# Kernel tuning notes

Measured on AMD Instinct MI355X. Metric: run time of the kernel, lower is better.

Reference implementation:

```python
import jax, jax.numpy as jnp
import numpy as np

K = 15          # n_clusters
D = 64          # dim_latent
M = 100         # number of w samples
LOG_2PI = float(np.log(2.0 * np.pi))

# state -> (cluster A, cluster B) edge endpoints, upper-triangular incl. diagonal
_A, _B = np.nonzero(np.triu(np.ones((K, K))))  # each [S], S = K*(K+1)/2 = 120


def setup_inputs() -> dict:
    key = jax.random.key(0)
    k1, k2, k3 = jax.random.split(key, 3)
    z = jax.random.normal(k1, (4096, 1, D), dtype=jnp.float32)      # [B, L, D]
    pi = jax.random.normal(k2, (1, K * (K + 1) // 2), dtype=jnp.float32)  # [1, S]
    mu = jax.random.uniform(k3, (D, K), dtype=jnp.float32, minval=-1.0, maxval=1.0)
    return {"z": z, "pi": pi, "mu": mu}


def reference(z, pi, mu):
    # w grid: [M]
    w = jnp.arange(M, dtype=z.dtype) / M
    # interpolated component means mu_sm[d, s, m] = mu[d,A[s]]*w[m] + mu[d,B[s]]*(1-w[m])
    mu_sm = mu[:, _A, None] * w + mu[:, _B, None] * (1.0 - w)   # [D, S, M]
    log_pi = jnp.log(jax.nn.softmax(pi, axis=-1) + 1e-30)       # [1, S]

    # squared distance via ||z||^2 - 2 z.mu + ||mu||^2 (avoids [B,L,D,S,M] materialization)
    zz = jnp.sum(z * z, axis=-1)                                # [B, L]
    cross = jnp.einsum('bld,dsm->blsm', z, mu_sm)               # [B, L, S, M]
    mm = jnp.sum(mu_sm * mu_sm, axis=0)                         # [S, M]
    sq = zz[..., None, None] - 2.0 * cross + mm                 # [B, L, S, M]

    log_p_zc_w = (-0.5 * D * LOG_2PI
                  + log_pi[0][None, None, :, None]
                  - 0.5 * sq)                                   # [B, L, S, M]
    log_p_z_L = jax.scipy.special.logsumexp(log_p_zc_w, axis=(2, 3))  # [B, L]
    log_p_z = jnp.mean(log_p_z_L) - jnp.log(jnp.asarray(M, z.dtype))
    return log_p_z
```

## Files before the change

### kernel.cpp

```cpp
#include <hip/hip_runtime.h>
#include <math.h>
#include <float.h>

#define D 64
#define K 15
#define S 120
#define MNUM 100
#define C0 (-58.81206612509905f)
#define L2E 1.4426950408889634f
#define INV_L2E 0.6931471805599453f

static __device__ __forceinline__ float fexp2(float x) {
    return __builtin_amdgcn_exp2f(x);
}


__global__ __launch_bounds__(128) void gmm_setup(const float* __restrict__ pi,
                                                 const float* __restrict__ mu,
                                                 float* __restrict__ wsf,
                                                 int* __restrict__ wsi) {
    __shared__ float red[2];
    __shared__ float bcast;
    const int t = threadIdx.x;
    const int wid = t >> 6;

    float p = (t < S) ? pi[t] : -FLT_MAX;
    float mx = p;
    for (int off = 32; off; off >>= 1) mx = fmaxf(mx, __shfl_down(mx, off));
    if ((t & 63) == 0) red[wid] = mx;
    __syncthreads();
    if (t == 0) bcast = fmaxf(red[0], red[1]);
    __syncthreads();
    mx = bcast;
    __syncthreads();

    float e = (t < S) ? __expf(p - mx) : 0.f;
    float se = e;
    for (int off = 32; off; off >>= 1) se += __shfl_down(se, off);
    if ((t & 63) == 0) red[wid] = se;
    __syncthreads();
    if (t == 0) bcast = red[0] + red[1];
    __syncthreads();
    se = bcast;

    if (t < S) {
        float sm = e / se;
        float logpi = logf(sm + 1e-30f);

        int i = 0, rem = t;
        while (rem >= K - i) { rem -= K - i; ++i; }
        int j = i + rem;

        float aa = 0.f, ab = 0.f, bb = 0.f;
        for (int d = 0; d < D; ++d) {
            float ma = mu[d * K + i];
            float mb = mu[d * K + j];
            aa = fmaf(ma, ma, aa);
            ab = fmaf(ma, mb, ab);
            bb = fmaf(mb, mb, bb);
        }
        float q0 = bb;
        float q1 = 2.f * (ab - bb);
        float q2 = aa - 2.f * ab + bb;

        wsf[t]       = C0 + logpi - 0.5f * q0;
        wsf[128 + t] = -0.5f * q1;
        wsf[256 + t] = -0.5f * q2;
        wsi[t]       = i;
        wsi[128 + t] = j;
    }
}

__global__ __launch_bounds__(256) void gmm_main(const float* __restrict__ z,
                                                const float* __restrict__ mu,
                                                const float* __restrict__ wsf,
                                                const int* __restrict__ wsi,
                                                float* __restrict__ lse) {
    __shared__ float zsh[4][D];
    const int t = threadIdx.x;
    const int lane = t & 63;
    const int wv = t >> 6;
    const int b = (blockIdx.x << 2) + wv;

    float zval = z[b * D + lane];
    zsh[wv][lane] = zval;
    float zz = zval * zval;
    #pragma unroll
    for (int off = 32; off; off >>= 1) zz += __shfl_xor(zz, off);
    __syncthreads();

    const int g = lane >> 4;
    const int kk = lane & 15;
    const int kkc = (kk < K) ? kk : (K - 1);
    const float* zw = &zsh[wv][g * 16];
    float cpart = 0.f;
    #pragma unroll
    for (int i = 0; i < 16; ++i)
        cpart = fmaf(zw[i], mu[(g * 16 + i) * K + kkc], cpart);
    cpart += __shfl_xor(cpart, 16);
    cpart += __shfl_xor(cpart, 32);

    const int s1 = lane;
    const int s2 = lane + 64;
    const bool v2 = (s2 < S);
    const int s2c = v2 ? s2 : (S - 1);

    float cA1 = __shfl(cpart, wsi[s1]);
    float cB1 = __shfl(cpart, wsi[128 + s1]);
    float cA2 = __shfl(cpart, wsi[s2c]);
    float cB2 = __shfl(cpart, wsi[128 + s2c]);

    float T01 = wsf[s1] + cB1 - 0.5f * zz;
    float T11 = wsf[128 + s1] + (cA1 - cB1);
    float T21 = wsf[256 + s1];
    float T02 = v2 ? (wsf[s2c] + cB2 - 0.5f * zz) : -1e30f;
    float T12 = wsf[128 + s2c] + (cA2 - cB2);
    float T22 = wsf[256 + s2c];

    float bnd = fmaxf(T01, fmaf(0.99f, fmaf(0.99f, T21, T11), T01));
    if (T21 < 0.f) {
        float wv1 = fminf(fmaxf(-T11 / (2.f * T21), 0.f), 0.99f);
        bnd = fmaxf(bnd, fmaf(wv1, fmaf(wv1, T21, T11), T01));
    }
    if (v2) {
        float b2 = fmaxf(T02, fmaf(0.99f, fmaf(0.99f, T22, T12), T02));
        if (T22 < 0.f) {
            float wv2 = fminf(fmaxf(-T12 / (2.f * T22), 0.f), 0.99f);
            b2 = fmaxf(b2, fmaf(wv2, fmaf(wv2, T22, T12), T02));
        }
        bnd = fmaxf(bnd, b2);
    }
    #pragma unroll
    for (int off = 32; off; off >>= 1) bnd = fmaxf(bnd, __shfl_xor(bnd, off));
    const float Mb = bnd;

    const float u01 = (T01 - Mb) * L2E, u11 = T11 * L2E, u21 = T21 * L2E;
    const float u02 = (T02 - Mb) * L2E, u12 = T12 * L2E, u22 = T22 * L2E;

    float sumA = 0.f, sumB = 0.f;
    float w = 0.f;
    #pragma unroll 10
    for (int m = 0; m < 100; ++m) {
        sumA += fexp2(fmaf(w, fmaf(w, u21, u11), u01));
        sumB += fexp2(fmaf(w, fmaf(w, u22, u12), u02));
        w += 0.01f;
    }
    float ssum = sumA + sumB;
    #pragma unroll
    for (int off = 32; off; off >>= 1) ssum += __shfl_xor(ssum, off);

    if (lane == 0)
        lse[b] = Mb + __builtin_amdgcn_logf(ssum) * INV_L2E;
}

__global__ __launch_bounds__(256) void gmm_reduce(const float* __restrict__ lse,
                                                  float* __restrict__ out) {
    __shared__ float red[4];
    const int t = threadIdx.x;
    float s = 0.f;
    #pragma unroll
    for (int i = 0; i < 16; ++i) s += lse[t + i * 256];
    #pragma unroll
    for (int off = 32; off; off >>= 1) s += __shfl_down(s, off);
    if ((t & 63) == 0) red[t >> 6] = s;
    __syncthreads();
    if (t == 0)
        out[0] = (red[0] + red[1] + red[2] + red[3]) * (1.0f / 4096.0f)
                 - logf((float)MNUM);
}

extern "C" void kernel_launch(void* const* d_in, const int* in_sizes, int n_in,
                              void* d_out, int out_size, void* d_ws, size_t ws_size,
                              hipStream_t stream) {
    const float* z  = (const float*)d_in[0];
    const float* pi = (const float*)d_in[1];
    const float* mu = (const float*)d_in[2];
    float* out = (float*)d_out;

    float* wsf = (float*)d_ws;
    int*   wsi = (int*)(wsf + 384);
    float* lse = wsf + 1024;

    gmm_setup<<<1, 128, 0, stream>>>(pi, mu, wsf, wsi);
    gmm_main<<<1024, 256, 0, stream>>>(z, mu, wsf, wsi, lse);
    gmm_reduce<<<1, 256, 0, stream>>>(lse, out);
}
```

Measured before the change: 72.58 us.

## Replace per-sample exp2 with multiplicative recurrence from grid midpoint

The 100 exp2 evaluations per state are replaced by a geometric recurrence: the Gaussian-in-w term is computed as products of precomputed ratio factors, stepping outward from w=0.5 in both directions, so only four exp2 calls per state remain. Division in the bound computation is replaced by a hardware reciprocal. This removes transcendental throughput cost from the inner loop but accumulates rounding error over 50 chained multiplies and may underflow or overflow for extreme exponents.

```diff
diff --git a/kernel.cpp b/kernel.cpp
--- a/kernel.cpp
+++ b/kernel.cpp
@@ -119,13 +119,13 @@
 
     float bnd = fmaxf(T01, fmaf(0.99f, fmaf(0.99f, T21, T11), T01));
     if (T21 < 0.f) {
-        float wv1 = fminf(fmaxf(-T11 / (2.f * T21), 0.f), 0.99f);
+        float wv1 = fminf(fmaxf(-T11 * 0.5f * __builtin_amdgcn_rcpf(T21), 0.f), 0.99f);
         bnd = fmaxf(bnd, fmaf(wv1, fmaf(wv1, T21, T11), T01));
     }
     if (v2) {
         float b2 = fmaxf(T02, fmaf(0.99f, fmaf(0.99f, T22, T12), T02));
         if (T22 < 0.f) {
-            float wv2 = fminf(fmaxf(-T12 / (2.f * T22), 0.f), 0.99f);
+            float wv2 = fminf(fmaxf(-T12 * 0.5f * __builtin_amdgcn_rcpf(T22), 0.f), 0.99f);
             b2 = fmaxf(b2, fmaf(wv2, fmaf(wv2, T22, T12), T02));
         }
         bnd = fmaxf(bnd, b2);
@@ -134,18 +134,34 @@
     for (int off = 32; off; off >>= 1) bnd = fmaxf(bnd, __shfl_xor(bnd, off));
     const float Mb = bnd;
 
-    const float u01 = (T01 - Mb) * L2E, u11 = T11 * L2E, u21 = T21 * L2E;
-    const float u02 = (T02 - Mb) * L2E, u12 = T12 * L2E, u22 = T22 * L2E;
-
-    float sumA = 0.f, sumB = 0.f;
-    float w = 0.f;
+    const float a01 = (T01 - Mb) * L2E, a11 = T11 * L2E, a21 = T21 * L2E;
+    const float a02 = (T02 - Mb) * L2E, a12 = T12 * L2E, a22 = T22 * L2E;
+
+    float e1  = fexp2(fmaf(0.5f, fmaf(0.5f, a21, a11), a01));
+    float g1  = fexp2(fmaf(0.0101f, a21,  0.01f * a11));
+    float dd1 = fexp2(fmaf(-0.0099f, a21, -0.01f * a11));
+    float h1  = fexp2(2.0e-4f * a21);
+
+    float e2  = fexp2(fmaf(0.5f, fmaf(0.5f, a22, a12), a02));
+    float g2  = fexp2(fmaf(0.0101f, a22,  0.01f * a12));
+    float dd2 = fexp2(fmaf(-0.0099f, a22, -0.01f * a12));
+    float h2  = fexp2(2.0e-4f * a22);
+
+    float eu1 = e1,        gu1 = g1;
+    float ed1 = e1 * dd1,  du1 = dd1 * h1;
+    float eu2 = e2,        gu2 = g2;
+    float ed2 = e2 * dd2,  du2 = dd2 * h2;
+    float su1 = 0.f, sd1 = 0.f, su2 = 0.f, sd2 = 0.f;
+
     #pragma unroll 10
-    for (int m = 0; m < 100; ++m) {
-        sumA += fexp2(fmaf(w, fmaf(w, u21, u11), u01));
-        sumB += fexp2(fmaf(w, fmaf(w, u22, u12), u02));
-        w += 0.01f;
-    }
-    float ssum = sumA + sumB;
+    for (int m = 0; m < 50; ++m) {
+        su1 += eu1; eu1 *= gu1; gu1 *= h1;
+        sd1 += ed1; ed1 *= du1; du1 *= h1;
+        su2 += eu2; eu2 *= gu2; gu2 *= h2;
+        sd2 += ed2; ed2 *= du2; du2 *= h2;
+    }
+
+    float ssum = (su1 + sd1) + (su2 + sd2);
     #pragma unroll
     for (int off = 32; off; off >>= 1) ssum += __shfl_xor(ssum, off);
 
```

Measured after the change: 69.04 us. -4.9%, faster.
